# Optimization experiments

Hardware: AMD Instinct MI355X
Metric: run time of the kernel (lower is better)

The kernel has to match this reference:

```python
import jax, jax.numpy as jnp
import numpy as np

CODE_NUM = 64
IN_FEATURES = 3
CODE_CHANNEL = 64
SHAPE_NUM = 16


def setup_inputs() -> dict:
    key = jax.random.key(0)
    k1, k2, k3 = jax.random.split(key, 3)
    B, P = 8, 65536
    coords = jax.random.uniform(k1, (B, P, IN_FEATURES), dtype=jnp.float32)  # in [0,1) subset of [-1,1]
    idx = jax.random.randint(k2, (B,), 0, SHAPE_NUM, dtype=jnp.int32)
    # xavier_uniform for [C, shape_num*F*code_num]
    fan_in = SHAPE_NUM * IN_FEATURES * CODE_NUM
    bound = float(np.sqrt(6.0 / (CODE_CHANNEL + fan_in)))
    shape_code = jax.random.uniform(k3, (CODE_CHANNEL, fan_in), dtype=jnp.float32,
                                    minval=-bound, maxval=bound)
    return {"coords": coords, "idx": idx, "shape_code": shape_code}


def reference(coords, idx, shape_code):
    # coords: [B, P, F] in [-1, 1]; idx: [B] int; shape_code: [C, S*F*code_num]
    B, P, F = coords.shape
    C = shape_code.shape[0]
    # map to grid coordinates in [0, code_num-1]
    g = (coords + 1.0) * ((CODE_NUM - 1) / 2.0)                    # [B,P,F]
    corners = jnp.floor(g)[..., None] + jnp.array([0.0, 1.0], g.dtype)  # [B,P,F,2]
    coordsf = g[..., None] - corners                               # [B,P,F,2]
    weights = 1.0 - jnp.abs(coordsf)                               # [B,P,F,2]
    # flat codebook index: corner + feature offset + per-batch shape offset
    feat_off = (CODE_NUM * jnp.arange(F, dtype=jnp.int32))[:, None]        # [F,1]
    shape_off = (idx.astype(jnp.int32) * (CODE_NUM * F))[:, None, None, None]  # [B,1,1,1]
    index = corners.astype(jnp.int32) + feat_off + shape_off       # [B,P,F,2]
    # gather [B,P,F,2,C] then weighted reduce over (F,2)
    code_t = shape_code.T                                          # [S*F*code_num, C]
    gathered = code_t[index]                                       # [B,P,F,2,C]
    output = jnp.einsum('bpfkc,bpfk->bpc', gathered, weights)      # [B,P,C]
    return output
```

## Files before the change

kernel.cpp:

```cpp
#include <hip/hip_runtime.h>


#define CODE_NUM 64
#define NFEAT 3
#define NCHAN 64
#define NB 8
#define NP 65536
#define SLICE (CODE_NUM * NFEAT)
#define ROW_STRIDE 3072
#define NTHREADS 512
#define BLOCKS_PER_BATCH 64
#define PTS_PER_BLOCK (NP / BLOCKS_PER_BATCH)
#define PTS_PER_ITER (NTHREADS / 16)

__global__ __launch_bounds__(NTHREADS)
void posenc_kernel(const float* __restrict__ coords,
                   const int* __restrict__ idx,
                   const float* __restrict__ shape_code,
                   float* __restrict__ out) {
    __shared__ float lds[SLICE * NCHAN];

    const int bx    = blockIdx.x;
    const int b     = bx >> 6;
    const int chunk = (bx & (BLOCKS_PER_BATCH - 1)) * PTS_PER_BLOCK;
    const int tid   = threadIdx.x;

    const int base = idx[b] * SLICE;

    {
        const int c      = tid & 63;
        const int jchunk = tid >> 6;
        const float* src = shape_code + (size_t)c * ROW_STRIDE + base;
        #pragma unroll
        for (int jv = jchunk; jv < SLICE / 4; jv += NTHREADS / 64) {
            const float4 v = *reinterpret_cast<const float4*>(src + jv * 4);
            lds[(jv * 4 + 0) * NCHAN + c] = v.x;
            lds[(jv * 4 + 1) * NCHAN + c] = v.y;
            lds[(jv * 4 + 2) * NCHAN + c] = v.z;
            lds[(jv * 4 + 3) * NCHAN + c] = v.w;
        }
    }
    __syncthreads();

    const int gl   = tid & 15;
    const int pofs = tid >> 4;
    const size_t bp0 = (size_t)b * NP;

    for (int it = 0; it < PTS_PER_BLOCK / PTS_PER_ITER; ++it) {
        const int p = chunk + it * PTS_PER_ITER + pofs;
        const float* cp = coords + (bp0 + p) * NFEAT;

        const float x0 = cp[0];
        const float x1 = cp[1];
        const float x2 = cp[2];

        float4 acc = make_float4(0.f, 0.f, 0.f, 0.f);

        #pragma unroll
        for (int f = 0; f < NFEAT; ++f) {
            const float xf = (f == 0) ? x0 : (f == 1) ? x1 : x2;
            const float g  = (xf + 1.0f) * ((CODE_NUM - 1) * 0.5f);
            int c0 = (int)floorf(g);
            c0 = max(0, min(c0, CODE_NUM - 2));
            const float w1 = g - (float)c0;
            const float w0 = 1.0f - w1;

            const int r = (f * CODE_NUM + c0) * NCHAN + gl * 4;
            const float4 v0 = *reinterpret_cast<const float4*>(&lds[r]);
            const float4 v1 = *reinterpret_cast<const float4*>(&lds[r + NCHAN]);

            acc.x = fmaf(w0, v0.x, fmaf(w1, v1.x, acc.x));
            acc.y = fmaf(w0, v0.y, fmaf(w1, v1.y, acc.y));
            acc.z = fmaf(w0, v0.z, fmaf(w1, v1.z, acc.z));
            acc.w = fmaf(w0, v0.w, fmaf(w1, v1.w, acc.w));
        }

        float4* op = reinterpret_cast<float4*>(out + (bp0 + p) * NCHAN + gl * 4);
        *op = acc;
    }
}

extern "C" void kernel_launch(void* const* d_in, const int* in_sizes, int n_in,
                              void* d_out, int out_size, void* d_ws, size_t ws_size,
                              hipStream_t stream) {
    const float* coords     = (const float*)d_in[0];
    const int*   idx        = (const int*)d_in[1];
    const float* shape_code = (const float*)d_in[2];
    float*       out        = (float*)d_out;

    dim3 grid(NB * BLOCKS_PER_BATCH);
    dim3 block(NTHREADS);
    posenc_kernel<<<grid, block, 0, stream>>>(coords, idx, shape_code, out);
}
```

Measured before the change: 177.8 us.

## Replace LDS codebook staging with pre-transposed global codebook read through cache

Adds a separate transpose kernel that writes the whole codebook channel-last into workspace, then drops the per-block LDS load and barrier. Each thread now reads its six float4 corner values directly from global memory, relying on L1/L2 caching of the small per-shape slice. Block size shrinks to 256 threads with four times more blocks and an occupancy hint. This removes the redundant per-block staging of 48KB, at the cost of an extra kernel launch, a transpose of the full codebook every call, and cache-dependent gathers.

```diff
diff --git a/kernel.cpp b/kernel.cpp
--- a/kernel.cpp
+++ b/kernel.cpp
@@ -8,75 +8,81 @@
 #define NP 65536
 #define SLICE (CODE_NUM * NFEAT)
 #define ROW_STRIDE 3072
-#define NTHREADS 512
-#define BLOCKS_PER_BATCH 64
+#define CODE_T_ELEMS (ROW_STRIDE * NCHAN)
+
+__global__ __launch_bounds__(256)
+void transpose_kernel(const float* __restrict__ shape_code,
+                      float* __restrict__ code_t) {
+    const int t = blockIdx.x * 256 + threadIdx.x;
+    const int c = t & 63;
+    const int j = t >> 6;
+    code_t[t] = shape_code[(size_t)c * ROW_STRIDE + j];
+}
+
+#define NTHREADS 256
+#define BLOCKS_PER_BATCH 256
 #define PTS_PER_BLOCK (NP / BLOCKS_PER_BATCH)
 #define PTS_PER_ITER (NTHREADS / 16)
+#define NIT (PTS_PER_BLOCK / PTS_PER_ITER)
 
-__global__ __launch_bounds__(NTHREADS)
+__global__ __launch_bounds__(NTHREADS, 6)
 void posenc_kernel(const float* __restrict__ coords,
                    const int* __restrict__ idx,
-                   const float* __restrict__ shape_code,
+                   const float* __restrict__ code_t,
                    float* __restrict__ out) {
-    __shared__ float lds[SLICE * NCHAN];
-
     const int bx    = blockIdx.x;
-    const int b     = bx >> 6;
+    const int b     = bx >> 8;
     const int chunk = (bx & (BLOCKS_PER_BATCH - 1)) * PTS_PER_BLOCK;
     const int tid   = threadIdx.x;
+    const int gl    = tid & 15;
+    const int pofs  = tid >> 4;
 
-    const int base = idx[b] * SLICE;
+    const size_t bp0 = (size_t)b * NP;
+    const float* cb0 = code_t + (size_t)idx[b] * (SLICE * NCHAN) + gl * 4;
+    const float* cb1 = cb0 + CODE_NUM * NCHAN;
+    const float* cb2 = cb1 + CODE_NUM * NCHAN;
+    const float* cp  = coords + (bp0 + chunk) * NFEAT;
+    float*       og  = out + (bp0 + chunk) * NCHAN + gl * 4;
 
-    {
-        const int c      = tid & 63;
-        const int jchunk = tid >> 6;
-        const float* src = shape_code + (size_t)c * ROW_STRIDE + base;
-        #pragma unroll
-        for (int jv = jchunk; jv < SLICE / 4; jv += NTHREADS / 64) {
-            const float4 v = *reinterpret_cast<const float4*>(src + jv * 4);
-            lds[(jv * 4 + 0) * NCHAN + c] = v.x;
-            lds[(jv * 4 + 1) * NCHAN + c] = v.y;
-            lds[(jv * 4 + 2) * NCHAN + c] = v.z;
-            lds[(jv * 4 + 3) * NCHAN + c] = v.w;
-        }
-    }
-    __syncthreads();
+    for (int it = 0; it < NIT; ++it) {
+        const int lp = it * PTS_PER_ITER + pofs;
 
-    const int gl   = tid & 15;
-    const int pofs = tid >> 4;
-    const size_t bp0 = (size_t)b * NP;
+        const float x0 = cp[lp * 3 + 0];
+        const float x1 = cp[lp * 3 + 1];
+        const float x2 = cp[lp * 3 + 2];
 
-    for (int it = 0; it < PTS_PER_BLOCK / PTS_PER_ITER; ++it) {
-        const int p = chunk + it * PTS_PER_ITER + pofs;
-        const float* cp = coords + (bp0 + p) * NFEAT;
+        const float g0 = fmaf(x0, 31.5f, 31.5f);
+        const float g1 = fmaf(x1, 31.5f, 31.5f);
+        const float g2 = fmaf(x2, 31.5f, 31.5f);
+        int i0 = (int)floorf(g0); i0 = max(0, min(i0, CODE_NUM - 2));
+        int i1 = (int)floorf(g1); i1 = max(0, min(i1, CODE_NUM - 2));
+        int i2 = (int)floorf(g2); i2 = max(0, min(i2, CODE_NUM - 2));
+        const float w1a = g0 - (float)i0, w0a = 1.0f - w1a;
+        const float w1b = g1 - (float)i1, w0b = 1.0f - w1b;
+        const float w1c = g2 - (float)i2, w0c = 1.0f - w1c;
 
-        const float x0 = cp[0];
-        const float x1 = cp[1];
-        const float x2 = cp[2];
+        const float4 a0 = *reinterpret_cast<const float4*>(cb0 + i0 * NCHAN);
+        const float4 a1 = *reinterpret_cast<const float4*>(cb0 + i0 * NCHAN + NCHAN);
+        const float4 b0 = *reinterpret_cast<const float4*>(cb1 + i1 * NCHAN);
+        const float4 b1 = *reinterpret_cast<const float4*>(cb1 + i1 * NCHAN + NCHAN);
+        const float4 c0 = *reinterpret_cast<const float4*>(cb2 + i2 * NCHAN);
+        const float4 c1 = *reinterpret_cast<const float4*>(cb2 + i2 * NCHAN + NCHAN);
 
-        float4 acc = make_float4(0.f, 0.f, 0.f, 0.f);
+        float4 acc;
+        acc.x = fmaf(w0a, a0.x, w1a * a1.x);
+        acc.y = fmaf(w0a, a0.y, w1a * a1.y);
+        acc.z = fmaf(w0a, a0.z, w1a * a1.z);
+        acc.w = fmaf(w0a, a0.w, w1a * a1.w);
+        acc.x = fmaf(w0b, b0.x, fmaf(w1b, b1.x, acc.x));
+        acc.y = fmaf(w0b, b0.y, fmaf(w1b, b1.y, acc.y));
+        acc.z = fmaf(w0b, b0.z, fmaf(w1b, b1.z, acc.z));
+        acc.w = fmaf(w0b, b0.w, fmaf(w1b, b1.w, acc.w));
+        acc.x = fmaf(w0c, c0.x, fmaf(w1c, c1.x, acc.x));
+        acc.y = fmaf(w0c, c0.y, fmaf(w1c, c1.y, acc.y));
+        acc.z = fmaf(w0c, c0.z, fmaf(w1c, c1.z, acc.z));
+        acc.w = fmaf(w0c, c0.w, fmaf(w1c, c1.w, acc.w));
 
-        #pragma unroll
-        for (int f = 0; f < NFEAT; ++f) {
-            const float xf = (f == 0) ? x0 : (f == 1) ? x1 : x2;
-            const float g  = (xf + 1.0f) * ((CODE_NUM - 1) * 0.5f);
-            int c0 = (int)floorf(g);
-            c0 = max(0, min(c0, CODE_NUM - 2));
-            const float w1 = g - (float)c0;
-            const float w0 = 1.0f - w1;
-
-            const int r = (f * CODE_NUM + c0) * NCHAN + gl * 4;
-            const float4 v0 = *reinterpret_cast<const float4*>(&lds[r]);
-            const float4 v1 = *reinterpret_cast<const float4*>(&lds[r + NCHAN]);
-
-            acc.x = fmaf(w0, v0.x, fmaf(w1, v1.x, acc.x));
-            acc.y = fmaf(w0, v0.y, fmaf(w1, v1.y, acc.y));
-            acc.z = fmaf(w0, v0.z, fmaf(w1, v1.z, acc.z));
-            acc.w = fmaf(w0, v0.w, fmaf(w1, v1.w, acc.w));
-        }
-
-        float4* op = reinterpret_cast<float4*>(out + (bp0 + p) * NCHAN + gl * 4);
-        *op = acc;
+        *reinterpret_cast<float4*>(og + (size_t)lp * NCHAN) = acc;
     }
 }
 
@@ -87,8 +93,11 @@
     const int*   idx        = (const int*)d_in[1];
     const float* shape_code = (const float*)d_in[2];
     float*       out        = (float*)d_out;
+    float*       code_t     = (float*)d_ws;
+
+    transpose_kernel<<<CODE_T_ELEMS / 256, 256, 0, stream>>>(shape_code, code_t);
 
     dim3 grid(NB * BLOCKS_PER_BATCH);
     dim3 block(NTHREADS);
-    posenc_kernel<<<grid, block, 0, stream>>>(coords, idx, shape_code, out);
+    posenc_kernel<<<grid, block, 0, stream>>>(coords, idx, code_t, out);
 }
```

Result: slower. 191.4 us (+7.7%).
